# Kernel optimization log

Measured on AMD Instinct MI355X. Metric: run time of the kernel, lower is better.

## Reference

```python
import jax, jax.numpy as jnp
import numpy as np

# Config constants derived from init_kwargs
VX, VY = 0.16, 0.16
X0, Y0 = 0.0, -39.68
X_OFF = VX / 2 + X0
Y_OFF = VY / 2 + Y0
X_L, Y_L = 432, 496  # round((x1-x0)/vx), round((y1-y0)/vy)
B = 4
C_OUT = 64
BN_EPS = 1e-3


def setup_inputs() -> dict:
    key = jax.random.key(0)
    ks = jax.random.split(key, 9)
    M, P = 64000, 32
    pillars = jax.random.normal(ks[0], (M, P, 4), dtype=jnp.float32)
    b_id = jax.random.randint(ks[1], (M,), 0, B, dtype=jnp.int32)
    z_id = jnp.zeros((M,), dtype=jnp.int32)
    y_id = jax.random.randint(ks[2], (M,), 0, Y_L, dtype=jnp.int32)
    x_id = jax.random.randint(ks[3], (M,), 0, X_L, dtype=jnp.int32)
    coors = jnp.stack([b_id, z_id, y_id, x_id], axis=1)
    nums = jax.random.randint(ks[4], (M,), 1, P + 1, dtype=jnp.int32)
    W = jax.random.normal(ks[5], (C_OUT, 9), dtype=jnp.float32) * 0.1
    gamma = 1.0 + 0.1 * jax.random.normal(ks[6], (C_OUT,), dtype=jnp.float32)
    beta = 0.1 * jax.random.normal(ks[7], (C_OUT,), dtype=jnp.float32)
    running_mean = 0.1 * jax.random.normal(ks[8], (C_OUT,), dtype=jnp.float32)
    running_var = jax.random.uniform(ks[8], (C_OUT,), dtype=jnp.float32, minval=0.5, maxval=1.5)
    return {"pillars": pillars, "coors": coors, "nums": nums, "W": W,
            "gamma": gamma, "beta": beta,
            "running_mean": running_mean, "running_var": running_var}


def reference(pillars, coors, nums, W, gamma, beta, running_mean, running_var):
    M, P, _ = pillars.shape
    numsf = nums.astype(jnp.float32)
    point_mask = (jnp.arange(P)[None, :] < nums[:, None]).astype(pillars.dtype)  # [M,P]

    # mean of valid xyz per pillar, center features
    masked_xyz = pillars[:, :, :3] * point_mask[:, :, None]
    mean = masked_xyz.sum(axis=1, keepdims=True) / jnp.clip(numsf, 1.0)[:, None, None]
    f_centered = pillars[:, :, :3] - mean

    # offsets from pillar center
    x_c = coors[:, 3].astype(jnp.float32) * VX + X_OFF
    y_c = coors[:, 2].astype(jnp.float32) * VY + Y_OFF
    f_x = pillars[:, :, 0:1] - x_c[:, None, None]
    f_y = pillars[:, :, 1:2] - y_c[:, None, None]

    features = jnp.concatenate([pillars, f_centered, f_x, f_y], axis=2)  # [M,P,9]
    features = features * point_mask[:, :, None]

    # 1x1 conv + eval-mode BN + ReLU, then max over points
    h = jnp.einsum('mpc,oc->mpo', features, W)  # [M,P,C_OUT]
    scale = gamma / jnp.sqrt(running_var + BN_EPS)
    h = jax.nn.relu(h * scale + (beta - running_mean * scale))
    pooled = h.max(axis=1)  # [M,C_OUT]

    b = coors[:, 0]
    y = coors[:, 2]
    x = coors[:, 3]
    valid = (x >= 0) & (x < X_L) & (y >= 0) & (y < Y_L)
    y_s = jnp.where(valid, y, Y_L)
    x_s = jnp.where(valid, x, X_L)
    canvas = jnp.zeros((B, Y_L, X_L, C_OUT), dtype=pooled.dtype)
    canvas = canvas.at[b, y_s, x_s].set(pooled, mode='drop')
    return canvas.transpose(0, 3, 1, 2)  # [B, C_OUT, Y_L, X_L]
```

## Files before the change

### kernel.cpp

```cpp
#include <hip/hip_runtime.h>

#define XL 432
#define YL 496
#define CELLS_B (YL * XL)
#define PLANE4 (CELLS_B / 4)
#define BN 4
#define COUT 64
#define PP 32
#define TCELLS 128
#define TG 32
#define LSTR 132

typedef float v4f __attribute__((ext_vector_type(4)));

__global__ __launch_bounds__(256) void winner_kernel(const int* __restrict__ coors,
                                                     int* __restrict__ winner, int M) {
    int m = blockIdx.x * blockDim.x + threadIdx.x;
    if (m >= M) return;
    const int4 c = ((const int4*)coors)[m];
    if (c.w < 0 || c.w >= XL || c.z < 0 || c.z >= YL) return;
    atomicMax(&winner[(c.x * YL + c.z) * XL + c.w], m);
}

__global__ __launch_bounds__(256) void pillar_compute(
    const float* __restrict__ pillars,
    const int* __restrict__ coors,
    const int* __restrict__ nums,
    const float* __restrict__ W,
    const float* __restrict__ gamma, const float* __restrict__ beta,
    const float* __restrict__ rmean, const float* __restrict__ rvar,
    const int* __restrict__ winner,
    float* __restrict__ pooled,
    int M) {
    const int pb   = threadIdx.x >> 6;
    const int lane = threadIdx.x & 63;
    const int m    = blockIdx.x * 4 + pb;

    __shared__ float4 pts[4][PP];

    if (m < M && lane < PP) {
        pts[pb][lane] = ((const float4*)pillars)[m * PP + lane];
    }
    __syncthreads();
    if (m >= M) return;

    const int4 co = ((const int4*)coors)[m];
    const int x = co.w, y = co.z;
    if (x < 0 || x >= XL || y < 0 || y >= YL) return;
    if (winner[(co.x * YL + y) * XL + x] != m) return;

    int num = nums[m];
    if (num < 1) num = 1;
    if (num > PP) num = PP;

    const float scale = gamma[lane] * rsqrtf(rvar[lane] + 1e-3f);
    const float bias  = beta[lane] - rmean[lane] * scale;

    const float w0 = W[lane * 9 + 0], w1 = W[lane * 9 + 1], w2 = W[lane * 9 + 2];
    const float w3 = W[lane * 9 + 3], w4 = W[lane * 9 + 4], w5 = W[lane * 9 + 5];
    const float w6 = W[lane * 9 + 6], w7 = W[lane * 9 + 7], w8 = W[lane * 9 + 8];
    const float cwx = w0 + w4 + w7, cwy = w1 + w5 + w8, cwz = w2 + w6, cww = w3;

    float sx = 0.f, sy = 0.f, sz = 0.f;
    float dmax = -3.0e38f, dmin = 3.0e38f;
    for (int p = 0; p < num; ++p) {
        const float4 q = pts[pb][p];
        sx += q.x; sy += q.y; sz += q.z;
        const float d = q.x * cwx + q.y * cwy + q.z * cwz + q.w * cww;
        dmax = fmaxf(dmax, d);
        dmin = fminf(dmin, d);
    }
    const float inv = 1.0f / (float)num;
    const float xc = (float)x * 0.16f + 0.08f;
    const float yc = (float)y * 0.16f + (0.08f - 39.68f);
    const float C0 = sx * inv * w4 + sy * inv * w5 + sz * inv * w6
                   + xc * w7 + yc * w8;

    const float sel = (scale >= 0.f) ? dmax : dmin;
    float v = (sel - C0) * scale + bias;
    if (num < PP) v = fmaxf(v, bias);
    pooled[m * COUT + lane] = fmaxf(v, 0.f);
}

__global__ __launch_bounds__(512) void canvas_kernel(
    const int* __restrict__ winner,
    const float* __restrict__ pooled,
    v4f* __restrict__ out4) {
    __shared__ float lds[COUT * LSTR];

    const int t   = threadIdx.x;
    const int b   = blockIdx.y;
    const int blk = blockIdx.x;
    const int baseCell = blk * TCELLS;

    {
        const int cell = t >> 2;
        const int qq   = t & 3;
        const int w = winner[b * CELLS_B + baseCell + cell];

        float4 r[4];
        if (w >= 0) {
            const float4* row = (const float4*)(pooled + (size_t)w * COUT);
            #pragma unroll
            for (int k = 0; k < 4; ++k) r[k] = row[qq + 4 * k];
        } else {
            #pragma unroll
            for (int k = 0; k < 4; ++k) r[k] = make_float4(0.f, 0.f, 0.f, 0.f);
        }
        #pragma unroll
        for (int k = 0; k < 4; ++k) {
            const int cb = 4 * (qq + 4 * k);
            lds[(cb + 0) * LSTR + cell] = r[k].x;
            lds[(cb + 1) * LSTR + cell] = r[k].y;
            lds[(cb + 2) * LSTR + cell] = r[k].z;
            lds[(cb + 3) * LSTR + cell] = r[k].w;
        }
    }
    __syncthreads();

    {
        const int xg  = t & 31;
        const int chi = t >> 5;
        v4f* outb = out4 + (size_t)b * COUT * PLANE4 + (size_t)blk * TG + xg;
        #pragma unroll
        for (int cc = 0; cc < 4; ++cc) {
            const int c = cc * 16 + chi;
            const v4f v = *(const v4f*)&lds[c * LSTR + 4 * xg];
            __builtin_nontemporal_store(v, &outb[(size_t)c * PLANE4]);
        }
    }
}

extern "C" void kernel_launch(void* const* d_in, const int* in_sizes, int n_in,
                              void* d_out, int out_size, void* d_ws, size_t ws_size,
                              hipStream_t stream) {
    const float* pillars = (const float*)d_in[0];
    const int*   coors   = (const int*)d_in[1];
    const int*   nums    = (const int*)d_in[2];
    const float* W       = (const float*)d_in[3];
    const float* gamma   = (const float*)d_in[4];
    const float* beta    = (const float*)d_in[5];
    const float* rmean   = (const float*)d_in[6];
    const float* rvar    = (const float*)d_in[7];
    float* out = (float*)d_out;

    const int M = in_sizes[2];
    int*   winner = (int*)d_ws;
    float* pooled = (float*)((char*)d_ws + (size_t)BN * CELLS_B * sizeof(int));

    (void)hipMemsetAsync(winner, 0xFF, (size_t)BN * CELLS_B * sizeof(int), stream);

    winner_kernel<<<(M + 255) / 256, 256, 0, stream>>>(coors, winner, M);
    pillar_compute<<<(M + 3) / 4, 256, 0, stream>>>(
        pillars, coors, nums, W, gamma, beta, rmean, rvar, winner, pooled, M);

    dim3 cgrid(CELLS_B / TCELLS, BN);
    canvas_kernel<<<cgrid, 512, 0, stream>>>(winner, pooled, (v4f*)out);
}
```

Measured before the change: 298.9 us.

## Make canvas kernel persistent with double-buffered LDS and prefetch of next tile

The canvas scatter kernel becomes a persistent grid of 768 blocks of 384 threads, each looping over 96-cell tiles. The next tile's winner index and pooled row are loaded while the current tile is written out, and two LDS buffers allow one barrier per iteration. The goal is to hide global load latency and cut block launch overhead for the large canvas write. The cost is more LDS and registers per block, and a loop that may limit occupancy.

```diff
diff --git a/kernel.cpp b/kernel.cpp
--- a/kernel.cpp
+++ b/kernel.cpp
@@ -7,9 +7,13 @@
 #define BN 4
 #define COUT 64
 #define PP 32
-#define TCELLS 128
-#define TG 32
-#define LSTR 132
+
+#define TCELLS 96
+#define TPB (CELLS_B / TCELLS)
+#define NTILES (BN * TPB)
+#define LSTR 100
+#define CTHREADS 384
+#define CBLOCKS 768
 
 typedef float v4f __attribute__((ext_vector_type(4)));
 
@@ -23,15 +27,11 @@
 }
 
 __global__ __launch_bounds__(256) void pillar_compute(
-    const float* __restrict__ pillars,
-    const int* __restrict__ coors,
-    const int* __restrict__ nums,
-    const float* __restrict__ W,
+    const float* __restrict__ pillars, const int* __restrict__ coors,
+    const int* __restrict__ nums, const float* __restrict__ W,
     const float* __restrict__ gamma, const float* __restrict__ beta,
     const float* __restrict__ rmean, const float* __restrict__ rvar,
-    const int* __restrict__ winner,
-    float* __restrict__ pooled,
-    int M) {
+    const int* __restrict__ winner, float* __restrict__ pooled, int M) {
     const int pb   = threadIdx.x >> 6;
     const int lane = threadIdx.x & 63;
     const int m    = blockIdx.x * 4 + pb;
@@ -82,52 +82,85 @@
     pooled[m * COUT + lane] = fmaxf(v, 0.f);
 }
 
-__global__ __launch_bounds__(512) void canvas_kernel(
+__global__ __launch_bounds__(CTHREADS) void canvas_kernel(
     const int* __restrict__ winner,
     const float* __restrict__ pooled,
     v4f* __restrict__ out4) {
-    __shared__ float lds[COUT * LSTR];
+    __shared__ float lds[2][COUT * LSTR];
 
-    const int t   = threadIdx.x;
-    const int b   = blockIdx.y;
-    const int blk = blockIdx.x;
-    const int baseCell = blk * TCELLS;
+    const int t0   = threadIdx.x;
+    const int cell = t0 >> 2;
+    const int qq   = t0 & 3;
+    const int chi  = t0 / 24;
+    const int xg   = t0 - chi * 24;
 
+    int t = blockIdx.x;
+    if (t >= NTILES) return;
+
+    auto widx = [&](int tt) {
+        int b = tt / TPB, ti = tt - b * TPB;
+        return b * CELLS_B + ti * TCELLS + cell;
+    };
+
+    int w_cur = winner[widx(t)];
+    int t1 = t + CBLOCKS;
+    int w_nxt = (t1 < NTILES) ? winner[widx(t1)] : -1;
+
+    float4 r[4];
     {
-        const int cell = t >> 2;
-        const int qq   = t & 3;
-        const int w = winner[b * CELLS_B + baseCell + cell];
-
-        float4 r[4];
-        if (w >= 0) {
-            const float4* row = (const float4*)(pooled + (size_t)w * COUT);
+        if (w_cur >= 0) {
+            const float4* row = (const float4*)(pooled + (size_t)w_cur * COUT);
             #pragma unroll
             for (int k = 0; k < 4; ++k) r[k] = row[qq + 4 * k];
         } else {
             #pragma unroll
             for (int k = 0; k < 4; ++k) r[k] = make_float4(0.f, 0.f, 0.f, 0.f);
         }
+    }
+
+    int buf = 0;
+    while (true) {
         #pragma unroll
         for (int k = 0; k < 4; ++k) {
             const int cb = 4 * (qq + 4 * k);
-            lds[(cb + 0) * LSTR + cell] = r[k].x;
-            lds[(cb + 1) * LSTR + cell] = r[k].y;
-            lds[(cb + 2) * LSTR + cell] = r[k].z;
-            lds[(cb + 3) * LSTR + cell] = r[k].w;
+            lds[buf][(cb + 0) * LSTR + cell] = r[k].x;
+            lds[buf][(cb + 1) * LSTR + cell] = r[k].y;
+            lds[buf][(cb + 2) * LSTR + cell] = r[k].z;
+            lds[buf][(cb + 3) * LSTR + cell] = r[k].w;
         }
-    }
-    __syncthreads();
 
-    {
-        const int xg  = t & 31;
-        const int chi = t >> 5;
-        v4f* outb = out4 + (size_t)b * COUT * PLANE4 + (size_t)blk * TG + xg;
+        const int t2 = t1 + CBLOCKS;
+        const int w2 = (t2 < NTILES) ? winner[widx(t2)] : -1;
+        const bool have_next = (t1 < NTILES);
+        float4 rn[4];
+        if (have_next && w_nxt >= 0) {
+            const float4* row = (const float4*)(pooled + (size_t)w_nxt * COUT);
+            #pragma unroll
+            for (int k = 0; k < 4; ++k) rn[k] = row[qq + 4 * k];
+        } else {
+            #pragma unroll
+            for (int k = 0; k < 4; ++k) rn[k] = make_float4(0.f, 0.f, 0.f, 0.f);
+        }
+
+        __syncthreads();
+
+        {
+            const int b = t / TPB, ti = t - b * TPB;
+            v4f* outb = out4 + (size_t)b * COUT * PLANE4 + (size_t)ti * (TCELLS / 4) + xg;
+            #pragma unroll
+            for (int cc = 0; cc < 4; ++cc) {
+                const int c = cc * 16 + chi;
+                const v4f v = *(const v4f*)&lds[buf][c * LSTR + 4 * xg];
+                __builtin_nontemporal_store(v, &outb[(size_t)c * PLANE4]);
+            }
+        }
+
+        if (!have_next) break;
+        t = t1; t1 = t2;
+        w_cur = w_nxt; w_nxt = w2;
         #pragma unroll
-        for (int cc = 0; cc < 4; ++cc) {
-            const int c = cc * 16 + chi;
-            const v4f v = *(const v4f*)&lds[c * LSTR + 4 * xg];
-            __builtin_nontemporal_store(v, &outb[(size_t)c * PLANE4]);
-        }
+        for (int k = 0; k < 4; ++k) r[k] = rn[k];
+        buf ^= 1;
     }
 }
 
@@ -154,6 +187,5 @@
     pillar_compute<<<(M + 3) / 4, 256, 0, stream>>>(
         pillars, coors, nums, W, gamma, beta, rmean, rvar, winner, pooled, M);
 
-    dim3 cgrid(CELLS_B / TCELLS, BN);
-    canvas_kernel<<<cgrid, 512, 0, stream>>>(winner, pooled, (v4f*)out);
+    canvas_kernel<<<CBLOCKS, CTHREADS, 0, stream>>>(winner, pooled, (v4f*)out);
 }
```

Measured after the change: 304.3 us. About the same (+1.8%).

## Split canvas transpose across channel groups with larger cell tiles

Applied to the files above, without the earlier changes.

The canvas kernel now runs one block per tile of 256 cells, per group of 8 channels, per batch, instead of one block covering 128 cells across all 64 channels. This shrinks LDS per block and raises the number of blocks, so more waves can be resident while writing the output. In exchange, each winner index is re-read once per channel group, and each thread gathers only 32 bytes from a pooled row, which makes the gather reads less coalesced.

```diff
diff --git a/kernel.cpp b/kernel.cpp
--- a/kernel.cpp
+++ b/kernel.cpp
@@ -7,9 +7,12 @@
 #define BN 4
 #define COUT 64
 #define PP 32
-#define TCELLS 128
-#define TG 32
-#define LSTR 132
+
+#define TCELLS 256
+#define TPB (CELLS_B / TCELLS)
+#define CG 8
+#define NCG (COUT / CG)
+#define LSTR 264
 
 typedef float v4f __attribute__((ext_vector_type(4)));
 
@@ -23,15 +26,11 @@
 }
 
 __global__ __launch_bounds__(256) void pillar_compute(
-    const float* __restrict__ pillars,
-    const int* __restrict__ coors,
-    const int* __restrict__ nums,
-    const float* __restrict__ W,
+    const float* __restrict__ pillars, const int* __restrict__ coors,
+    const int* __restrict__ nums, const float* __restrict__ W,
     const float* __restrict__ gamma, const float* __restrict__ beta,
     const float* __restrict__ rmean, const float* __restrict__ rvar,
-    const int* __restrict__ winner,
-    float* __restrict__ pooled,
-    int M) {
+    const int* __restrict__ winner, float* __restrict__ pooled, int M) {
     const int pb   = threadIdx.x >> 6;
     const int lane = threadIdx.x & 63;
     const int m    = blockIdx.x * 4 + pb;
@@ -82,52 +81,49 @@
     pooled[m * COUT + lane] = fmaxf(v, 0.f);
 }
 
-__global__ __launch_bounds__(512) void canvas_kernel(
+__global__ __launch_bounds__(256) void canvas_kernel(
     const int* __restrict__ winner,
     const float* __restrict__ pooled,
     v4f* __restrict__ out4) {
-    __shared__ float lds[COUT * LSTR];
+    __shared__ float lds[CG * LSTR];
 
-    const int t   = threadIdx.x;
-    const int b   = blockIdx.y;
-    const int blk = blockIdx.x;
-    const int baseCell = blk * TCELLS;
+    const int tile = blockIdx.x;
+    const int cg   = blockIdx.y;
+    const int b    = blockIdx.z;
+    const int t    = threadIdx.x;
 
     {
-        const int cell = t >> 2;
-        const int qq   = t & 3;
-        const int w = winner[b * CELLS_B + baseCell + cell];
-
-        float4 r[4];
+        const int cell = t;
+        const int w = winner[b * CELLS_B + tile * TCELLS + cell];
+        float4 r0, r1;
         if (w >= 0) {
-            const float4* row = (const float4*)(pooled + (size_t)w * COUT);
-            #pragma unroll
-            for (int k = 0; k < 4; ++k) r[k] = row[qq + 4 * k];
+            const float4* row = (const float4*)(pooled + (size_t)w * COUT + cg * CG);
+            r0 = row[0];
+            r1 = row[1];
         } else {
-            #pragma unroll
-            for (int k = 0; k < 4; ++k) r[k] = make_float4(0.f, 0.f, 0.f, 0.f);
+            r0 = make_float4(0.f, 0.f, 0.f, 0.f);
+            r1 = make_float4(0.f, 0.f, 0.f, 0.f);
         }
-        #pragma unroll
-        for (int k = 0; k < 4; ++k) {
-            const int cb = 4 * (qq + 4 * k);
-            lds[(cb + 0) * LSTR + cell] = r[k].x;
-            lds[(cb + 1) * LSTR + cell] = r[k].y;
-            lds[(cb + 2) * LSTR + cell] = r[k].z;
-            lds[(cb + 3) * LSTR + cell] = r[k].w;
-        }
+        lds[0 * LSTR + cell] = r0.x;
+        lds[1 * LSTR + cell] = r0.y;
+        lds[2 * LSTR + cell] = r0.z;
+        lds[3 * LSTR + cell] = r0.w;
+        lds[4 * LSTR + cell] = r1.x;
+        lds[5 * LSTR + cell] = r1.y;
+        lds[6 * LSTR + cell] = r1.z;
+        lds[7 * LSTR + cell] = r1.w;
     }
     __syncthreads();
 
     {
+        const int chi = t >> 5;
         const int xg  = t & 31;
-        const int chi = t >> 5;
-        v4f* outb = out4 + (size_t)b * COUT * PLANE4 + (size_t)blk * TG + xg;
-        #pragma unroll
-        for (int cc = 0; cc < 4; ++cc) {
-            const int c = cc * 16 + chi;
-            const v4f v = *(const v4f*)&lds[c * LSTR + 4 * xg];
-            __builtin_nontemporal_store(v, &outb[(size_t)c * PLANE4]);
-        }
+        const int c   = cg * CG + chi;
+        v4f* outp = out4 + (size_t)(b * COUT + c) * PLANE4 + (size_t)tile * (TCELLS / 4);
+        const v4f v0 = *(const v4f*)&lds[chi * LSTR + 4 * xg];
+        const v4f v1 = *(const v4f*)&lds[chi * LSTR + 4 * (xg + 32)];
+        __builtin_nontemporal_store(v0, &outp[xg]);
+        __builtin_nontemporal_store(v1, &outp[xg + 32]);
     }
 }
 
@@ -154,6 +150,6 @@
     pillar_compute<<<(M + 3) / 4, 256, 0, stream>>>(
         pillars, coors, nums, W, gamma, beta, rmean, rvar, winner, pooled, M);
 
-    dim3 cgrid(CELLS_B / TCELLS, BN);
-    canvas_kernel<<<cgrid, 512, 0, stream>>>(winner, pooled, (v4f*)out);
+    dim3 cgrid(TPB, NCG, BN);
+    canvas_kernel<<<cgrid, 256, 0, stream>>>(winner, pooled, (v4f*)out);
 }
```

Result: no change. 297.4 us (-0.5%).
